# Optimization experiments

Hardware: AMD Instinct MI355X
Metric: run time of the kernel (lower is better)

The kernel has to match this reference:

```python
import jax, jax.numpy as jnp
import numpy as np

NEG_INF = -1e30  # stand-in for -inf that is safe under fp16/bf16 softmax


def setup_inputs() -> dict:
    key = jax.random.key(0)
    k1, k2, k3, k4 = jax.random.split(key, 4)
    B, T, C, H = 4, 4096, 1024, 64
    x = jax.random.normal(k1, (B, T, C), dtype=jnp.float32)
    Wq = jax.random.normal(k2, (C, H), dtype=jnp.float32) * (C ** -0.5)
    Wk = jax.random.normal(k3, (C, H), dtype=jnp.float32) * (C ** -0.5)
    Wv = jax.random.normal(k4, (C, H), dtype=jnp.float32) * (C ** -0.5)
    return {"x": x, "Wq": Wq, "Wk": Wk, "Wv": Wv}


def reference(x, Wq, Wk, Wv):
    # x: [B,T,C]; Wq/Wk/Wv: [C,H]
    q = jnp.einsum('btc,ch->bth', x, Wq)
    k = jnp.einsum('btc,ch->bth', x, Wk)
    v = jnp.einsum('btc,ch->bth', x, Wv)
    # NOTE: original module applies NO 1/sqrt(head_size) scaling — faithful here.
    wei = jnp.einsum('bqh,bkh->bqk', q, k)  # [B,T,T]
    T = x.shape[1]
    causal = jnp.tril(jnp.ones((T, T), dtype=bool))
    wei = jnp.where(causal, wei, NEG_INF)
    wei = jax.nn.softmax(wei, axis=-1)
    # dropout: eval-mode identity
    out = jnp.einsum('bqk,bkh->bqh', wei, v)  # [B,T,H]
    return out
```

## Files before the change

### kernel.cpp

```cpp
#include <hip/hip_runtime.h>
#include <hip/hip_fp16.h>


typedef __attribute__((ext_vector_type(8))) short bf16x8;
typedef __attribute__((ext_vector_type(8))) unsigned short u16x8;
typedef __attribute__((ext_vector_type(4))) float f32x4;

__device__ __forceinline__ unsigned short f2bf(float f) {
  unsigned u = __float_as_uint(f);
  u += 0x7fffu + ((u >> 16) & 1u);
  return (unsigned short)(u >> 16);
}
__device__ __forceinline__ float bf2f(unsigned short s) {
  return __uint_as_float(((unsigned)s) << 16);
}
__device__ __forceinline__ unsigned cvt_pk_bf16(float lo, float hi) {
  unsigned r;
  asm("v_cvt_pk_bf16_f32 %0, %1, %2" : "=v"(r) : "v"(lo), "v"(hi));
  return r;
}
__device__ __forceinline__ void gload_lds16(const void* g, void* l) {
  __builtin_amdgcn_global_load_lds(
      (const __attribute__((address_space(1))) unsigned int*)g,
      (__attribute__((address_space(3))) unsigned int*)l, 16, 0, 0);
}
#define KSWZ(row, colb) ((((row) * 128) + (colb)) ^ (((row) & 7) << 4))

__global__ __launch_bounds__(256) void wsplit_kernel(
    const float* __restrict__ Wq, const float* __restrict__ Wk,
    const float* __restrict__ Wv,
    unsigned short* __restrict__ Wth, unsigned short* __restrict__ Wtl) {
  const int fl = blockIdx.x * 256 + threadIdx.x;
  const int lane = fl & 63;
  const int rest = fl >> 6;
  const int nf = rest % 12;
  const int ksq = rest / 12;
  const int n = nf * 16 + (lane & 15);
  const int k0 = ksq * 32 + (lane >> 4) * 8;
  const float* wp = (n < 64) ? Wq : ((n < 128) ? Wk : Wv);
  const int h = n & 63;
  u16x8 hi, lo;
#pragma unroll
  for (int j = 0; j < 8; ++j) {
    float v = wp[(size_t)(k0 + j) * 64 + h];
    unsigned short hh = f2bf(v);
    hi[j] = hh;
    lo[j] = f2bf(v - bf2f(hh));
  }
  const size_t base = (size_t)fl * 8;
  *reinterpret_cast<u16x8*>(&Wth[base]) = hi;
  *reinterpret_cast<u16x8*>(&Wtl[base]) = lo;
}

__device__ __forceinline__ void cvt_store8(unsigned short* dh, unsigned short* dl,
                                           const float4& a, const float4& b) {
  float v[8] = {a.x, a.y, a.z, a.w, b.x, b.y, b.z, b.w};
  uint4 hp, lp;
  unsigned* hpp = reinterpret_cast<unsigned*>(&hp);
  unsigned* lpp = reinterpret_cast<unsigned*>(&lp);
#pragma unroll
  for (int p = 0; p < 4; ++p) {
    const unsigned h = cvt_pk_bf16(v[2 * p], v[2 * p + 1]);
    hpp[p] = h;
    const float h0 = __uint_as_float(h << 16);
    const float h1 = __uint_as_float(h & 0xffff0000u);
    lpp[p] = cvt_pk_bf16(v[2 * p] - h0, v[2 * p + 1] - h1);
  }
  *reinterpret_cast<uint4*>(dh) = hp;
  *reinterpret_cast<uint4*>(dl) = lp;
}

__global__ __launch_bounds__(256) void proj_mfma_kernel(
    const float* __restrict__ x,
    const unsigned short* __restrict__ Wth, const unsigned short* __restrict__ Wtl,
    unsigned short* __restrict__ qh, unsigned short* __restrict__ ql,
    unsigned short* __restrict__ kh, unsigned short* __restrict__ kl,
    unsigned short* __restrict__ vt) {
  __shared__ unsigned short Ah[2][32][72];
  __shared__ unsigned short Al[2][32][72];
  const int tid = threadIdx.x;
  const int w = tid >> 6;
  const int lane = tid & 63;
  const int l16 = lane & 15;
  const int g = lane >> 4;
  const int row0 = blockIdx.x * 32;
  const int sr = tid >> 3;
  const int sc = (tid & 7) * 8;

  f32x4 acc[2][3];
#pragma unroll
  for (int m = 0; m < 2; ++m)
#pragma unroll
    for (int f = 0; f < 3; ++f) {
      f32x4 z = {0.f, 0.f, 0.f, 0.f};
      acc[m][f] = z;
    }

  const float* xp = &x[(size_t)(row0 + sr) * 1024 + sc];

  float4 x0a = *reinterpret_cast<const float4*>(xp);
  float4 x0b = *reinterpret_cast<const float4*>(xp + 4);
  float4 x1a = *reinterpret_cast<const float4*>(xp + 64);
  float4 x1b = *reinterpret_cast<const float4*>(xp + 68);
  cvt_store8(&Ah[0][sr][sc], &Al[0][sr][sc], x0a, x0b);

  bf16x8 bhc[2][3], blc[2][3];
#pragma unroll
  for (int ks = 0; ks < 2; ++ks)
#pragma unroll
    for (int f = 0; f < 3; ++f) {
      const size_t off = ((size_t)ks * 12 + (w * 3 + f)) * 512 + lane * 8;
      bhc[ks][f] = *reinterpret_cast<const bf16x8*>(&Wth[off]);
      blc[ks][f] = *reinterpret_cast<const bf16x8*>(&Wtl[off]);
    }

#pragma unroll 2
  for (int step = 0; step < 16; ++step) {
    __syncthreads();
    bf16x8 bhn[2][3], bln[2][3];
    if (step < 15) {
#pragma unroll
      for (int ks = 0; ks < 2; ++ks)
#pragma unroll
        for (int f = 0; f < 3; ++f) {
          const size_t off =
              ((size_t)((step + 1) * 2 + ks) * 12 + (w * 3 + f)) * 512 + lane * 8;
          bhn[ks][f] = *reinterpret_cast<const bf16x8*>(&Wth[off]);
          bln[ks][f] = *reinterpret_cast<const bf16x8*>(&Wtl[off]);
        }
    }
    if (step < 14) {
      const float* px = xp + (size_t)(step + 2) * 64;
      if ((step & 1) == 0) {
        x0a = *reinterpret_cast<const float4*>(px);
        x0b = *reinterpret_cast<const float4*>(px + 4);
      } else {
        x1a = *reinterpret_cast<const float4*>(px);
        x1b = *reinterpret_cast<const float4*>(px + 4);
      }
    }
    const int cur = step & 1;
#pragma unroll
    for (int ks = 0; ks < 2; ++ks) {
      bf16x8 ah[2], al[2];
#pragma unroll
      for (int m = 0; m < 2; ++m) {
        const int ro = m * 16 + l16;
        const int co = ks * 32 + g * 8;
        ah[m] = *reinterpret_cast<const bf16x8*>(&Ah[cur][ro][co]);
        al[m] = *reinterpret_cast<const bf16x8*>(&Al[cur][ro][co]);
      }
#pragma unroll
      for (int m = 0; m < 2; ++m)
#pragma unroll
        for (int f = 0; f < 3; ++f) {
          acc[m][f] = __builtin_amdgcn_mfma_f32_16x16x32_bf16(ah[m], bhc[ks][f], acc[m][f], 0, 0, 0);
          acc[m][f] = __builtin_amdgcn_mfma_f32_16x16x32_bf16(ah[m], blc[ks][f], acc[m][f], 0, 0, 0);
          acc[m][f] = __builtin_amdgcn_mfma_f32_16x16x32_bf16(al[m], bhc[ks][f], acc[m][f], 0, 0, 0);
        }
    }
    if (step < 15) {
      if (((step + 1) & 1) == 0)
        cvt_store8(&Ah[cur ^ 1][sr][sc], &Al[cur ^ 1][sr][sc], x0a, x0b);
      else
        cvt_store8(&Ah[cur ^ 1][sr][sc], &Al[cur ^ 1][sr][sc], x1a, x1b);
    }
#pragma unroll
    for (int ks = 0; ks < 2; ++ks)
#pragma unroll
      for (int f = 0; f < 3; ++f) {
        bhc[ks][f] = bhn[ks][f];
        blc[ks][f] = bln[ks][f];
      }
  }

  const int b = row0 >> 12;
  const int tbase = row0 & 4095;
#pragma unroll
  for (int m = 0; m < 2; ++m)
#pragma unroll
    for (int f = 0; f < 3; ++f) {
      const int nn = w * 48 + f * 16;
      if (nn < 64) {
        const int h = nn + l16;
#pragma unroll
        for (int j = 0; j < 4; ++j) {
          const int row = row0 + m * 16 + 4 * g + j;
          const float val = acc[m][f][j];
          const unsigned short hi = f2bf(val);
          qh[(size_t)row * 64 + h] = hi;
          ql[(size_t)row * 64 + h] = f2bf(val - bf2f(hi));
        }
      } else if (nn < 128) {
        const int h = nn - 64 + l16;
#pragma unroll
        for (int j = 0; j < 4; ++j) {
          const int row = row0 + m * 16 + 4 * g + j;
          const float val = acc[m][f][j];
          const unsigned short hi = f2bf(val);
          kh[(size_t)row * 64 + h] = hi;
          kl[(size_t)row * 64 + h] = f2bf(val - bf2f(hi));
        }
      } else {
        const int h = nn - 128 + l16;
        ushort4 pv;
        pv.x = f2bf(acc[m][f][0]);
        pv.y = f2bf(acc[m][f][1]);
        pv.z = f2bf(acc[m][f][2]);
        pv.w = f2bf(acc[m][f][3]);
        const size_t a = ((size_t)b * 64 + h) * 4096 + tbase + m * 16 + 4 * g;
        *reinterpret_cast<ushort4*>(&vt[a]) = pv;
      }
    }
}

template <int PT, int NU_B>
__global__ __launch_bounds__(256) void attn_part_block_kernel(
    const unsigned short* __restrict__ qh, const unsigned short* __restrict__ ql,
    const unsigned short* __restrict__ kh, const unsigned short* __restrict__ kl,
    const unsigned short* __restrict__ vt,
    __half* __restrict__ OP, float* __restrict__ ML) {
  __shared__ __align__(16) unsigned short Khs[4096];
  __shared__ __align__(16) unsigned short Kls[4096];
  __shared__ __align__(16) unsigned short Vs[4096];
  __shared__ __align__(16) unsigned short pbuf[4][2][16][88];
  const int tid = threadIdx.x;
  const int w = tid >> 6;
  const int lane = tid & 63;
  const int l16 = lane & 15;
  const int g = lane >> 4;

  const int bx = blockIdx.x;
  const int xc = bx & 7;
  const int b = xc >> 1;
  const int s = 2 * (bx >> 3) + (xc & 1);
  int k = 0, pref = 0;
  for (;;) {
    const int np = (2 * k + 2 + PT - 1) / PT;
    if (s < pref + np) break;
    pref += np;
    ++k;
  }
  const int j4 = k;
  const int p = s - pref;
  const int ntiles = 2 * j4 + 2;
  const int t0 = p * PT;
  const int t1 = min(ntiles, t0 + PT);
  const int q0 = j4 * 128 + w * 32;
  const size_t rowbase = (size_t)b * 4096;

  bf16x8 q0hf[2], q0lf[2], q1hf[2], q1lf[2];
#pragma unroll
  for (int ss = 0; ss < 2; ++ss) {
    size_t a0 = (rowbase + q0 + l16) * 64 + ss * 32 + g * 8;
    q0hf[ss] = *reinterpret_cast<const bf16x8*>(&qh[a0]);
    q0lf[ss] = *reinterpret_cast<const bf16x8*>(&ql[a0]);
    size_t a1 = a0 + 16 * 64;
    q1hf[ss] = *reinterpret_cast<const bf16x8*>(&qh[a1]);
    q1lf[ss] = *reinterpret_cast<const bf16x8*>(&ql[a1]);
  }

  f32x4 o0[4], o1[4];
#pragma unroll
  for (int hb = 0; hb < 4; ++hb) {
    f32x4 z = {0.f, 0.f, 0.f, 0.f};
    o0[hb] = z;
    o1[hb] = z;
  }
  float m0 = -1e30f, l0 = 0.f, m1 = -1e30f, l1 = 0.f;

  for (int t = t0; t < t1; ++t) {
    const int kv0 = t * 64;
#pragma unroll
    for (int half = 0; half < 2; ++half) {
      const int te = half * 256 + w * 64 + lane;
      const int r = te >> 3;
      const int c8 = (te & 7) ^ (r & 7);
      const int ldsoff = half * 4096 + w * 1024 + lane * 16;
      gload_lds16(&kh[(rowbase + kv0 + r) * 64 + c8 * 8], (char*)Khs + ldsoff);
      gload_lds16(&kl[(rowbase + kv0 + r) * 64 + c8 * 8], (char*)Kls + ldsoff);
      gload_lds16(&vt[((size_t)b * 64 + r) * 4096 + kv0 + c8 * 8], (char*)Vs + ldsoff);
    }
    __syncthreads();

    f32x4 s0[4], s1[4];
#pragma unroll
    for (int kb = 0; kb < 4; ++kb) {
      bf16x8 khf[2], klf[2];
#pragma unroll
      for (int ss = 0; ss < 2; ++ss) {
        const int row = kb * 16 + l16;
        const int colb = ss * 64 + g * 16;
        khf[ss] = *reinterpret_cast<const bf16x8*>((const char*)Khs + KSWZ(row, colb));
        klf[ss] = *reinterpret_cast<const bf16x8*>((const char*)Kls + KSWZ(row, colb));
      }
      f32x4 a0 = {0.f, 0.f, 0.f, 0.f};
      f32x4 a1 = {0.f, 0.f, 0.f, 0.f};
#pragma unroll
      for (int ss = 0; ss < 2; ++ss) {
        a0 = __builtin_amdgcn_mfma_f32_16x16x32_bf16(khf[ss], q0hf[ss], a0, 0, 0, 0);
        a0 = __builtin_amdgcn_mfma_f32_16x16x32_bf16(khf[ss], q0lf[ss], a0, 0, 0, 0);
        a0 = __builtin_amdgcn_mfma_f32_16x16x32_bf16(klf[ss], q0hf[ss], a0, 0, 0, 0);
        a1 = __builtin_amdgcn_mfma_f32_16x16x32_bf16(khf[ss], q1hf[ss], a1, 0, 0, 0);
        a1 = __builtin_amdgcn_mfma_f32_16x16x32_bf16(khf[ss], q1lf[ss], a1, 0, 0, 0);
        a1 = __builtin_amdgcn_mfma_f32_16x16x32_bf16(klf[ss], q1hf[ss], a1, 0, 0, 0);
      }
      s0[kb] = a0;
      s1[kb] = a1;
    }
    bf16x8 vf[2][4];
#pragma unroll
    for (int ks = 0; ks < 2; ++ks)
#pragma unroll
      for (int hb = 0; hb < 4; ++hb) {
        const int row = hb * 16 + l16;
        const int colb = ks * 64 + g * 16;
        vf[ks][hb] = *reinterpret_cast<const bf16x8*>((const char*)Vs + KSWZ(row, colb));
      }
    if (kv0 + 63 > q0) {
#pragma unroll
      for (int kb = 0; kb < 4; ++kb)
#pragma unroll
        for (int jj = 0; jj < 4; ++jj) {
          const int kvg = kv0 + kb * 16 + 4 * g + jj;
          if (kvg > q0 + l16) s0[kb][jj] = -1e30f;
          if (kvg > q0 + 16 + l16) s1[kb][jj] = -1e30f;
        }
    }
    float rm0 = s0[0][0], rm1 = s1[0][0];
#pragma unroll
    for (int kb = 0; kb < 4; ++kb) {
      float c0 = fmaxf(fmaxf(s0[kb][0], s0[kb][1]), fmaxf(s0[kb][2], s0[kb][3]));
      float c1 = fmaxf(fmaxf(s1[kb][0], s1[kb][1]), fmaxf(s1[kb][2], s1[kb][3]));
      rm0 = fmaxf(rm0, c0);
      rm1 = fmaxf(rm1, c1);
    }
    rm0 = fmaxf(rm0, __shfl_xor(rm0, 16));
    rm0 = fmaxf(rm0, __shfl_xor(rm0, 32));
    rm1 = fmaxf(rm1, __shfl_xor(rm1, 16));
    rm1 = fmaxf(rm1, __shfl_xor(rm1, 32));
    const bool r0 = !__all(rm0 - m0 <= 8.f);
    const bool r1 = !__all(rm1 - m1 <= 8.f);
    const float mu0 = r0 ? fmaxf(m0, rm0) : m0;
    const float mu1 = r1 ? fmaxf(m1, rm1) : m1;
    const float al0 = r0 ? __expf(m0 - mu0) : 1.f;
    const float al1 = r1 ? __expf(m1 - mu1) : 1.f;
    float ps0 = 0.f, ps1 = 0.f;
#pragma unroll
    for (int kb = 0; kb < 4; ++kb)
#pragma unroll
      for (int jj = 0; jj < 4; ++jj) {
        const float e0 = __expf(s0[kb][jj] - mu0);
        const float e1 = __expf(s1[kb][jj] - mu1);
        s0[kb][jj] = e0;
        s1[kb][jj] = e1;
        ps0 += e0;
        ps1 += e1;
      }
    ps0 += __shfl_xor(ps0, 16);
    ps0 += __shfl_xor(ps0, 32);
    ps1 += __shfl_xor(ps1, 16);
    ps1 += __shfl_xor(ps1, 32);
    l0 = l0 * al0 + ps0;
    m0 = mu0;
    l1 = l1 * al1 + ps1;
    m1 = mu1;
#pragma unroll
    for (int kb = 0; kb < 4; ++kb) {
      *reinterpret_cast<unsigned*>(&pbuf[w][0][l16][kb * 16 + 4 * g]) =
          cvt_pk_bf16(s0[kb][0], s0[kb][1]);
      *reinterpret_cast<unsigned*>(&pbuf[w][0][l16][kb * 16 + 4 * g + 2]) =
          cvt_pk_bf16(s0[kb][2], s0[kb][3]);
      *reinterpret_cast<unsigned*>(&pbuf[w][1][l16][kb * 16 + 4 * g]) =
          cvt_pk_bf16(s1[kb][0], s1[kb][1]);
      *reinterpret_cast<unsigned*>(&pbuf[w][1][l16][kb * 16 + 4 * g + 2]) =
          cvt_pk_bf16(s1[kb][2], s1[kb][3]);
    }
    if (r0) {
#pragma unroll
      for (int jj = 0; jj < 4; ++jj) {
        const float a0r = __shfl(al0, 4 * g + jj);
#pragma unroll
        for (int hb = 0; hb < 4; ++hb) o0[hb][jj] *= a0r;
      }
    }
    if (r1) {
#pragma unroll
      for (int jj = 0; jj < 4; ++jj) {
        const float a1r = __shfl(al1, 4 * g + jj);
#pragma unroll
        for (int hb = 0; hb < 4; ++hb) o1[hb][jj] *= a1r;
      }
    }
    asm volatile("s_waitcnt lgkmcnt(0)" ::: "memory");
#pragma unroll
    for (int ks = 0; ks < 2; ++ks) {
      bf16x8 pa0 = *reinterpret_cast<const bf16x8*>(&pbuf[w][0][l16][ks * 32 + g * 8]);
      bf16x8 pa1 = *reinterpret_cast<const bf16x8*>(&pbuf[w][1][l16][ks * 32 + g * 8]);
#pragma unroll
      for (int hb = 0; hb < 4; ++hb) {
        o0[hb] = __builtin_amdgcn_mfma_f32_16x16x32_bf16(pa0, vf[ks][hb], o0[hb], 0, 0, 0);
        o1[hb] = __builtin_amdgcn_mfma_f32_16x16x32_bf16(pa1, vf[ks][hb], o1[hb], 0, 0, 0);
      }
    }
    __syncthreads();
  }

  const size_t u = (size_t)b * NU_B + s;
  __half* op = OP + u * 8192 + (size_t)w * 32 * 64;
#pragma unroll
  for (int jj = 0; jj < 4; ++jj) {
    const int srcr = 4 * g + jj;
    const float l0r = __shfl(l0, srcr);
    const float l1r = __shfl(l1, srcr);
#pragma unroll
    for (int hb = 0; hb < 4; ++hb) {
      op[(4 * g + jj) * 64 + hb * 16 + l16] = __float2half(o0[hb][jj] / l0r);
      op[(16 + 4 * g + jj) * 64 + hb * 16 + l16] = __float2half(o1[hb][jj] / l1r);
    }
  }
  float* ml = ML + u * 256 + w * 64;
  if (lane < 16) {
    ml[lane] = m0;
    ml[32 + lane] = l0;
  } else if (lane < 32) {
    ml[lane] = m1;
    ml[32 + lane] = l1;
  }
}

template <int PT, int NU_B>
__global__ __launch_bounds__(256) void attn_combine_kernel(
    const __half* __restrict__ OP, const float* __restrict__ ML,
    float* __restrict__ out) {
  const int tid = threadIdx.x;
  const int w = tid >> 6;
  const int lane = tid & 63;
  const int rid = blockIdx.x * 4 + w;
  const int b = rid >> 12;
  const int rr = rid & 4095;
  const int j4 = rr >> 7;
  const int local = rr & 127;
  const int nparts = (2 * j4 + 2 + PT - 1) / PT;
  int prefix = 0;
  for (int k = 0; k < j4; ++k) prefix += (2 * k + 2 + PT - 1) / PT;
  const size_t base = (size_t)b * NU_B + prefix;
  const int wv = local >> 5;
  const int tile = (local >> 4) & 1;
  const int rowin = local & 15;
  const int mi = wv * 64 + tile * 16 + rowin;

  float M = -1e30f;
  for (int p = 0; p < nparts; ++p) M = fmaxf(M, ML[(base + p) * 256 + mi]);
  float wsum = 0.f, acc = 0.f;
  for (int p = 0; p < nparts; ++p) {
    const float m = ML[(base + p) * 256 + mi];
    const float l = ML[(base + p) * 256 + 32 + mi];
    const float wg = l * __expf(m - M);
    wsum += wg;
    acc += wg * __half2float(OP[(base + p) * 8192 + (size_t)local * 64 + lane]);
  }
  out[(size_t)rid * 64 + lane] = acc / wsum;
}

extern "C" void kernel_launch(void* const* d_in, const int* in_sizes, int n_in,
                              void* d_out, int out_size, void* d_ws, size_t ws_size,
                              hipStream_t stream) {
  const float* x  = (const float*)d_in[0];
  const float* Wq = (const float*)d_in[1];
  const float* Wk = (const float*)d_in[2];
  const float* Wv = (const float*)d_in[3];
  float* out = (float*)d_out;

  const size_t N = (size_t)4 * 4096 * 64;
  const size_t WN = (size_t)192 * 1024;
  unsigned short* qh = (unsigned short*)d_ws;
  unsigned short* ql = qh + N;
  unsigned short* kh = ql + N;
  unsigned short* kl = kh + N;
  unsigned short* vt = kl + N;
  unsigned short* Wth = vt + N;
  unsigned short* Wtl = Wth + WN;
  __half* OP = (__half*)(Wtl + WN);
  const size_t base_need = (5 * N + 2 * WN) * 2;

  const size_t NU4 = 4 * 272, NU8 = 4 * 144;
  const size_t need4 = base_need + NU4 * 8192 * 2 + NU4 * 256 * 4;
  const size_t need8 = base_need + NU8 * 8192 * 2 + NU8 * 256 * 4;

  wsplit_kernel<<<dim3(96), dim3(256), 0, stream>>>(Wq, Wk, Wv, Wth, Wtl);
  proj_mfma_kernel<<<dim3(512), dim3(256), 0, stream>>>(x, Wth, Wtl, qh, ql, kh, kl, vt);
  if (ws_size >= need4) {
    float* ML = (float*)(OP + NU4 * 8192);
    attn_part_block_kernel<4, 272><<<dim3(NU4), dim3(256), 0, stream>>>(qh, ql, kh, kl, vt, OP, ML);
    attn_combine_kernel<4, 272><<<dim3(4096), dim3(256), 0, stream>>>(OP, ML, out);
  } else {
    float* ML = (float*)(OP + NU8 * 8192);
    attn_part_block_kernel<8, 144><<<dim3(NU8), dim3(256), 0, stream>>>(qh, ql, kh, kl, vt, OP, ML);
    attn_combine_kernel<8, 144><<<dim3(4096), dim3(256), 0, stream>>>(OP, ML, out);
  }
}
```

Baseline: 92.85 us.

## Double-buffer K/V LDS tiles to prefetch next tile during compute

Result: no change. 92.54 us (-0.3%).

```diff
diff --git a/kernel.cpp b/kernel.cpp
--- a/kernel.cpp
+++ b/kernel.cpp
@@ -220,9 +220,9 @@
     const unsigned short* __restrict__ kh, const unsigned short* __restrict__ kl,
     const unsigned short* __restrict__ vt,
     __half* __restrict__ OP, float* __restrict__ ML) {
-  __shared__ __align__(16) unsigned short Khs[4096];
-  __shared__ __align__(16) unsigned short Kls[4096];
-  __shared__ __align__(16) unsigned short Vs[4096];
+  __shared__ __align__(16) unsigned short Khs[2][4096];
+  __shared__ __align__(16) unsigned short Kls[2][4096];
+  __shared__ __align__(16) unsigned short Vs[2][4096];
   __shared__ __align__(16) unsigned short pbuf[4][2][16][88];
   const int tid = threadIdx.x;
   const int w = tid >> 6;
@@ -249,6 +249,12 @@
   const int q0 = j4 * 128 + w * 32;
   const size_t rowbase = (size_t)b * 4096;
 
+  const int te0 = w * 64 + lane;
+  const int te1 = 256 + w * 64 + lane;
+  const int r0_ = te0 >> 3, c80 = (te0 & 7) ^ (r0_ & 7);
+  const int r1_ = te1 >> 3, c81 = (te1 & 7) ^ (r1_ & 7);
+  const int lo0 = te0 * 16, lo1 = te1 * 16;
+
   bf16x8 q0hf[2], q0lf[2], q1hf[2], q1lf[2];
 #pragma unroll
   for (int ss = 0; ss < 2; ++ss) {
@@ -269,19 +275,29 @@
   }
   float m0 = -1e30f, l0 = 0.f, m1 = -1e30f, l1 = 0.f;
 
+  {
+    const int kv0 = t0 * 64;
+    gload_lds16(&kh[(rowbase + kv0 + r0_) * 64 + c80 * 8], (char*)Khs[0] + lo0);
+    gload_lds16(&kl[(rowbase + kv0 + r0_) * 64 + c80 * 8], (char*)Kls[0] + lo0);
+    gload_lds16(&vt[((size_t)b * 64 + r0_) * 4096 + kv0 + c80 * 8], (char*)Vs[0] + lo0);
+    gload_lds16(&kh[(rowbase + kv0 + r1_) * 64 + c81 * 8], (char*)Khs[0] + lo1);
+    gload_lds16(&kl[(rowbase + kv0 + r1_) * 64 + c81 * 8], (char*)Kls[0] + lo1);
+    gload_lds16(&vt[((size_t)b * 64 + r1_) * 4096 + kv0 + c81 * 8], (char*)Vs[0] + lo1);
+  }
+
+  int cur = 0;
   for (int t = t0; t < t1; ++t) {
+    __syncthreads();
+    if (t + 1 < t1) {
+      const int kn = (t + 1) * 64;
+      gload_lds16(&kh[(rowbase + kn + r0_) * 64 + c80 * 8], (char*)Khs[cur ^ 1] + lo0);
+      gload_lds16(&kl[(rowbase + kn + r0_) * 64 + c80 * 8], (char*)Kls[cur ^ 1] + lo0);
+      gload_lds16(&vt[((size_t)b * 64 + r0_) * 4096 + kn + c80 * 8], (char*)Vs[cur ^ 1] + lo0);
+      gload_lds16(&kh[(rowbase + kn + r1_) * 64 + c81 * 8], (char*)Khs[cur ^ 1] + lo1);
+      gload_lds16(&kl[(rowbase + kn + r1_) * 64 + c81 * 8], (char*)Kls[cur ^ 1] + lo1);
+      gload_lds16(&vt[((size_t)b * 64 + r1_) * 4096 + kn + c81 * 8], (char*)Vs[cur ^ 1] + lo1);
+    }
     const int kv0 = t * 64;
-#pragma unroll
-    for (int half = 0; half < 2; ++half) {
-      const int te = half * 256 + w * 64 + lane;
-      const int r = te >> 3;
-      const int c8 = (te & 7) ^ (r & 7);
-      const int ldsoff = half * 4096 + w * 1024 + lane * 16;
-      gload_lds16(&kh[(rowbase + kv0 + r) * 64 + c8 * 8], (char*)Khs + ldsoff);
-      gload_lds16(&kl[(rowbase + kv0 + r) * 64 + c8 * 8], (char*)Kls + ldsoff);
-      gload_lds16(&vt[((size_t)b * 64 + r) * 4096 + kv0 + c8 * 8], (char*)Vs + ldsoff);
-    }
-    __syncthreads();
 
     f32x4 s0[4], s1[4];
 #pragma unroll
@@ -291,8 +307,8 @@
       for (int ss = 0; ss < 2; ++ss) {
         const int row = kb * 16 + l16;
         const int colb = ss * 64 + g * 16;
-        khf[ss] = *reinterpret_cast<const bf16x8*>((const char*)Khs + KSWZ(row, colb));
-        klf[ss] = *reinterpret_cast<const bf16x8*>((const char*)Kls + KSWZ(row, colb));
+        khf[ss] = *reinterpret_cast<const bf16x8*>((const char*)Khs[cur] + KSWZ(row, colb));
+        klf[ss] = *reinterpret_cast<const bf16x8*>((const char*)Kls[cur] + KSWZ(row, colb));
       }
       f32x4 a0 = {0.f, 0.f, 0.f, 0.f};
       f32x4 a1 = {0.f, 0.f, 0.f, 0.f};
@@ -315,7 +331,7 @@
       for (int hb = 0; hb < 4; ++hb) {
         const int row = hb * 16 + l16;
         const int colb = ks * 64 + g * 16;
-        vf[ks][hb] = *reinterpret_cast<const bf16x8*>((const char*)Vs + KSWZ(row, colb));
+        vf[ks][hb] = *reinterpret_cast<const bf16x8*>((const char*)Vs[cur] + KSWZ(row, colb));
       }
     if (kv0 + 63 > q0) {
 #pragma unroll
@@ -403,7 +419,7 @@
         o1[hb] = __builtin_amdgcn_mfma_f32_16x16x32_bf16(pa1, vf[ks][hb], o1[hb], 0, 0, 0);
       }
     }
-    __syncthreads();
+    cur ^= 1;
   }
 
   const size_t u = (size_t)b * NU_B + s;
```
